# Kernel tuning notes

Measured on AMD Instinct MI355X. Metric: run time of the kernel, lower is better.

Reference implementation:

```python
import jax, jax.numpy as jnp
import numpy as np

P = 8          # patch_num_in == patch_num_out
R = 16         # patch_resolution (pixels per patch side)
C = 2          # dim_channel
D = 512        # dim_token
NH = 8         # nhead
DFF = 2048     # dim_feedforward
L = 6          # num_layers
PAIRS = 5      # demo_num
BS = 8
HW = P * R     # 128
S = PAIRS * 2 * P * P  # 640 tokens
EPS = 1e-5


def _patchify(x):
    # x: (N, c, H, W) -> (N, P*P, c*R*R)
    N, c, H, W = x.shape
    x = x.reshape(N, c, P, R, P, R).transpose(0, 2, 4, 1, 3, 5)
    return x.reshape(N, P * P, c * R * R)


def _depatchify(x, c):
    # x: (N, P*P, c*R*R) -> (N, c, P*R, P*R)
    N = x.shape[0]
    x = x.reshape(N, P, P, c, R, R).transpose(0, 3, 1, 4, 2, 5)
    return x.reshape(N, c, P * R, P * R)


def _ln(x, s, b):
    mu = jnp.mean(x, axis=-1, keepdims=True)
    var = jnp.mean(jnp.square(x - mu), axis=-1, keepdims=True)
    return (x - mu) * jax.lax.rsqrt(var + EPS) * s + b


def _block_lowtri_additive_mask(seq_len):
    blk = jnp.arange(seq_len) // (P * P)  # alternating init/end blocks of size P*P
    allowed = blk[:, None] >= blk[None, :]
    return jnp.where(allowed, 0.0, -jnp.inf).astype(jnp.float32)


def setup_inputs() -> dict:
    key = jax.random.key(0)
    ks = jax.random.split(key, 20)
    s = 0.02
    f32 = jnp.float32
    inp = {
        "init": jax.random.normal(ks[0], (BS, PAIRS, C, HW, HW), f32),
        "end": jax.random.normal(ks[1], (BS, PAIRS, C, HW, HW), f32),
        "c_mask": jnp.ones((BS, C), dtype=bool),
        "pre_W": (jax.random.normal(ks[2], (D, C * R * R), f32) * s),
        "pre_b": jnp.zeros((D,), f32),
        "post_W": (jax.random.normal(ks[3], (C * R * R, D), f32) * s),
        "post_b": jnp.zeros((C * R * R,), f32),
        "patch_pos": jax.random.normal(ks[4], (P * P, D), f32),
        "func_pos": jax.random.normal(ks[5], (PAIRS * 2, D), f32),
        "Wqkv": (jax.random.normal(ks[6], (L, 3 * D, D), f32) * s),
        "bqkv": jnp.zeros((L, 3 * D), f32),
        "Wo": (jax.random.normal(ks[7], (L, D, D), f32) * s),
        "bo": jnp.zeros((L, D), f32),
        "ln1_s": jnp.ones((L, D), f32),
        "ln1_b": jnp.zeros((L, D), f32),
        "ln2_s": jnp.ones((L, D), f32),
        "ln2_b": jnp.zeros((L, D), f32),
        "W1": (jax.random.normal(ks[8], (L, DFF, D), f32) * s),
        "b1": jnp.zeros((L, DFF), f32),
        "W2": (jax.random.normal(ks[9], (L, D, DFF), f32) * s),
        "b2": jnp.zeros((L, D), f32),
    }
    return inp


def _forward(init, end, pre_W, pre_b, post_W, post_b, patch_pos, func_pos,
             Wqkv, bqkv, Wo, bo, ln1_s, ln1_b, ln2_s, ln2_b, W1, b1, W2, b2):
    bs, pairs = init.shape[0], init.shape[1]
    # interleave (init, end) per pair: (bs, pairs, 2, c, h, w)
    x = jnp.concatenate([init[:, :, None], end[:, :, None]], axis=2)
    f = x.reshape(-1, C, HW, HW)
    f = _patchify(f)                                    # (N, P*P, C*R*R)
    f = f @ pre_W.T + pre_b                             # (N, P*P, D)
    f = f + patch_pos                                   # patch pos encoding
    f = f.reshape(bs, pairs * 2, P * P, D)
    f = f + func_pos[: pairs * 2][None, :, None, :]     # func pos encoding
    seq = pairs * 2 * P * P
    f = f.reshape(bs, seq, D)

    amask = _block_lowtri_additive_mask(seq)            # (S, S) additive
    dh = D // NH
    scale = 1.0 / np.sqrt(dh).astype(np.float32)

    for l in range(L):
        qkv = f @ Wqkv[l].T + bqkv[l]                   # (bs, S, 3D)
        q, k, v = jnp.split(qkv, 3, axis=-1)
        q = q.reshape(bs, seq, NH, dh).transpose(0, 2, 1, 3)
        k = k.reshape(bs, seq, NH, dh).transpose(0, 2, 1, 3)
        v = v.reshape(bs, seq, NH, dh).transpose(0, 2, 1, 3)
        scores = jnp.einsum('bhqd,bhkd->bhqk', q, k) * scale + amask
        attn = jax.nn.softmax(scores, axis=-1)
        o = jnp.einsum('bhqk,bhkd->bhqd', attn, v)
        o = o.transpose(0, 2, 1, 3).reshape(bs, seq, D)
        o = o @ Wo[l].T + bo[l]
        f = _ln(f + o, ln1_s[l], ln1_b[l])              # post-norm (PyTorch default)
        ff = jax.nn.gelu(f @ W1[l].T + b1[l], approximate=False) @ W2[l].T + b2[l]
        f = _ln(f + ff, ln2_s[l], ln2_b[l])

    f = f.reshape(bs, pairs, 2, P * P, D)[:, :, 0]      # read prediction off init slots
    f = f @ post_W.T + post_b                           # (bs, pairs, P*P, C*R*R)
    f = f.reshape(bs * pairs, P * P, C * R * R)
    f = _depatchify(f, C)
    return f.reshape(bs, pairs, C, HW, HW)


def reference(init, end, c_mask, pre_W, pre_b, post_W, post_b, patch_pos, func_pos,
              Wqkv, bqkv, Wo, bo, ln1_s, ln1_b, ln2_s, ln2_b, W1, b1, W2, b2):
    # c_mask is unpacked but unused by the original forward
    return _forward(init, end, pre_W, pre_b, post_W, post_b, patch_pos, func_pos,
                    Wqkv, bqkv, Wo, bo, ln1_s, ln1_b, ln2_s, ln2_b, W1, b1, W2, b2)
```

## Files before the change

kernel.cpp:

```cpp
#include <hip/hip_runtime.h>
#include <hip/hip_bf16.h>

#define BSZ 8
#define PAIRS 5
#define NCH 2
#define HWP 128
#define PP 64
#define DIM 512
#define NHEAD 8
#define DHEAD 64
#define DFF 2048
#define NLAYER 6
#define SEQ 640
#define NTOK (BSZ * SEQ)
#define FIN 10
#define MPOST (BSZ * PAIRS * PP)

typedef unsigned short u16;
typedef __bf16 bf16_t;
typedef __attribute__((ext_vector_type(8))) __bf16 bf16x8;
typedef __attribute__((ext_vector_type(8))) unsigned short u16x8;
typedef __attribute__((ext_vector_type(4))) unsigned short u16x4;
typedef __attribute__((ext_vector_type(4))) float f32x4;
#define MFMA16(a, b, c) __builtin_amdgcn_mfma_f32_16x16x32_bf16(a, b, c, 0, 0, 0)

__device__ __forceinline__ u16 f2b(float x) {
  unsigned u = __float_as_uint(x);
  return (u16)((u + 0x7fffu + ((u >> 16) & 1u)) >> 16);
}

__device__ __forceinline__ float gelu_t(float x) {
  float y = 0.7978845608f * (x + 0.044715f * x * x * x);
  y = fminf(fmaxf(y, -10.f), 10.f);
  float e = __expf(2.f * y);
  return 0.5f * x * (1.f + (e - 1.f) / (e + 1.f));
}

__device__ __forceinline__ void dma16(const u16* g, void* l) {
  __builtin_amdgcn_global_load_lds(
      (const __attribute__((address_space(1))) void*)g,
      (__attribute__((address_space(3))) void*)l, 16, 0, 0);
}

#define W_QKV (3 * DIM * DIM)
#define W_O (DIM * DIM)
#define W_1 (DFF * DIM)
#define OFF_O W_QKV
#define OFF_1 (W_QKV + W_O)
#define OFF_2 (W_QKV + W_O + W_1)
#define W_ALL (W_QKV + W_O + 2 * W_1)
#define PREPOST (2 * DIM * DIM)
#define N_CVT (PREPOST + NLAYER * W_ALL)

__global__ __launch_bounds__(256) void k_cvt_all(const float* __restrict__ preW,
                                                 const float* __restrict__ postW,
                                                 const float* __restrict__ wq,
                                                 const float* __restrict__ wo,
                                                 const float* __restrict__ w1,
                                                 const float* __restrict__ w2,
                                                 u16* __restrict__ dst) {
  size_t i = ((size_t)blockIdx.x * 256 + threadIdx.x) * 8;
  const float* src;
  size_t off;
  if (i < DIM * DIM) { src = preW; off = i; }
  else if (i < PREPOST) { src = postW; off = i - DIM * DIM; }
  else {
    size_t j = i - PREPOST;
    int l = (int)(j / W_ALL);
    size_t r = j - (size_t)l * W_ALL;
    if (r < OFF_O) { src = wq + (size_t)l * W_QKV; off = r; }
    else if (r < OFF_1) { src = wo + (size_t)l * W_O; off = r - OFF_O; }
    else if (r < OFF_2) { src = w1 + (size_t)l * W_1; off = r - OFF_1; }
    else { src = w2 + (size_t)l * W_1; off = r - OFF_2; }
  }
  float4 v0 = *(const float4*)(src + off);
  float4 v1 = *(const float4*)(src + off + 4);
  u16x8 o;
  o[0] = f2b(v0.x); o[1] = f2b(v0.y); o[2] = f2b(v0.z); o[3] = f2b(v0.w);
  o[4] = f2b(v1.x); o[5] = f2b(v1.y); o[6] = f2b(v1.z); o[7] = f2b(v1.w);
  *(u16x8*)(dst + i) = o;
}

__global__ __launch_bounds__(256) void k_patchify(const float* __restrict__ init,
                                                  const float* __restrict__ endp,
                                                  u16* __restrict__ A) {
  int i = blockIdx.x * 256 + threadIdx.x;
  int d = i & 511;
  int g = i >> 9;
  int p = g & 63;
  int fi = (g >> 6) % FIN;
  int b = g / SEQ;
  int e = fi & 1;
  int pr = fi >> 1;
  int c = d >> 8;
  int r1 = (d >> 4) & 15;
  int r2 = d & 15;
  int row = ((p >> 3) << 4) + r1;
  int col = ((p & 7) << 4) + r2;
  const float* src = e ? endp : init;
  size_t off = ((size_t)((b * PAIRS + pr) * NCH + c) << 14) + (size_t)row * HWP + col;
  A[i] = f2b(src[off]);
}

template <int BM, int NT, int MODE, int GATHER>
__global__ __launch_bounds__(256) void k_mma(const u16* __restrict__ A,
                                             const u16* __restrict__ B,
                                             const float* __restrict__ bias,
                                             u16* __restrict__ outB,
                                             float* __restrict__ outP,
                                             float* __restrict__ outF,
                                             const float* __restrict__ pp,
                                             const float* __restrict__ fp,
                                             int M, int N, int K, int act) {
  constexpr int FJ = NT / 32;
  constexpr int MI = BM / 32;
  constexpr int ACH = BM / 16;
  constexpr int NC = (BM / 16 + NT / 16) / 4;
  __shared__ __align__(16) bf16_t As[3][BM][32];
  __shared__ __align__(16) bf16_t Bs[3][NT][32];
  const int t = threadIdx.x;
  const int w = t >> 6, lane = t & 63, quad = lane >> 4, l16 = lane & 15;
  int bx = blockIdx.x, by = blockIdx.y;
  if ((gridDim.y & 7) == 0) {
    int lin = bx + gridDim.x * by;
    int YT = gridDim.y >> 3;
    int xcd = lin & 7, slot = lin >> 3;
    by = xcd * YT + slot % YT;
    bx = slot / YT;
  }
  const int row0 = by * BM, col0 = bx * NT;
  const int mB = (w & 1) * (BM / 2);
  const int nB = (w >> 1) * (NT / 2);

  const u16* aP[ACH];
#pragma unroll
  for (int c = 0; c < ACH; ++c) {
    int r = row0 + c * 16 + (lane >> 2);
    int g = r;
    if (GATHER) {
      int p = r & 63, pr = (r >> 6) % PAIRS, b = r / (PAIRS * PP);
      g = b * SEQ + pr * 128 + p;
    }
    aP[c] = A + (size_t)g * K + ((lane & 3) << 3);
  }
  const u16* bP = B + (size_t)(col0 + (lane >> 2)) * K + ((lane & 3) << 3);

  f32x4 acc[MI][FJ];
#pragma unroll
  for (int i = 0; i < MI; ++i)
#pragma unroll
    for (int j = 0; j < FJ; ++j) acc[i][j] = (f32x4){0.f, 0.f, 0.f, 0.f};

  auto stage = [&](int bu, int kk) {
#pragma unroll
    for (int s = 0; s < NC; ++s) {
      int c = NC * w + s;
      if (c < ACH) dma16(aP[c] + kk, &As[bu][c * 16][0]);
      else dma16(bP + (size_t)((c - ACH) * 16) * K + kk, &Bs[bu][(c - ACH) * 16][0]);
    }
  };

  const int iters = K >> 5;
  stage(0, 0);
  stage(1, 32);
  for (int it = 0; it < iters; ++it) {
    const int cur = it % 3;
    if (it > 0) asm volatile("s_barrier" ::: "memory");
    if (it + 2 < iters) stage((it + 2) % 3, (it + 2) << 5);
    if (it + 2 < iters) {
      if constexpr (NC == 2) asm volatile("s_waitcnt vmcnt(4)" ::: "memory");
      else if constexpr (NC == 3) asm volatile("s_waitcnt vmcnt(6)" ::: "memory");
      else asm volatile("s_waitcnt vmcnt(8)" ::: "memory");
    } else if (it + 1 < iters) {
      if constexpr (NC == 2) asm volatile("s_waitcnt vmcnt(2)" ::: "memory");
      else if constexpr (NC == 3) asm volatile("s_waitcnt vmcnt(3)" ::: "memory");
      else asm volatile("s_waitcnt vmcnt(4)" ::: "memory");
    } else {
      asm volatile("s_waitcnt vmcnt(0)" ::: "memory");
    }
    asm volatile("s_barrier" ::: "memory");
    bf16x8 af[MI], bfr[FJ];
#pragma unroll
    for (int i = 0; i < MI; ++i)
      af[i] = *(const bf16x8*)&As[cur][mB + i * 16 + l16][quad * 8];
#pragma unroll
    for (int j = 0; j < FJ; ++j)
      bfr[j] = *(const bf16x8*)&Bs[cur][nB + j * 16 + l16][quad * 8];
#pragma unroll
    for (int i = 0; i < MI; ++i)
#pragma unroll
      for (int j = 0; j < FJ; ++j) acc[i][j] = MFMA16(af[i], bfr[j], acc[i][j]);
  }

#pragma unroll
  for (int i = 0; i < MI; ++i)
#pragma unroll
    for (int reg = 0; reg < 4; ++reg) {
      int m = row0 + mB + i * 16 + quad * 4 + reg;
#pragma unroll
      for (int j = 0; j < FJ; ++j) {
        int n = col0 + nB + j * 16 + l16;
        float v = acc[i][j][reg];
        if (MODE == 0) {
          v += bias[n];
          if (act) v = gelu_t(v);
          outB[(size_t)m * N + n] = f2b(v);
        } else if (MODE == 1) {
          outP[(size_t)m * N + n] = v;
        } else if (MODE == 2) {
          int p = m & 63, fi = (m >> 6) % FIN;
          v += bias[n] + pp[p * DIM + n] + fp[fi * DIM + n];
          outF[(size_t)m * N + n] = v;
          outB[(size_t)m * N + n] = f2b(v);
        } else {
          v += bias[n];
          int p = m & 63, pr = (m >> 6) % PAIRS, b = m / (PAIRS * PP);
          int c = n >> 8, r1 = (n >> 4) & 15, r2 = n & 15;
          int row = ((p >> 3) << 4) + r1, col = ((p & 7) << 4) + r2;
          size_t off = ((size_t)((b * PAIRS + pr) * NCH + c) << 14) +
                       (size_t)row * HWP + col;
          outF[off] = v;
        }
      }
    }
}

__global__ __launch_bounds__(256) void k_attn(const u16* __restrict__ qkv,
                                              u16* __restrict__ o, int qmul) {
  __shared__ bf16_t Qs[64][72];
  __shared__ bf16_t Ks[64][72];
  __shared__ bf16_t Vs[64][72];
  __shared__ bf16_t Ps[64][72];
  const int t = threadIdx.x;
  const int w = t >> 6, lane = t & 63, quad = lane >> 4, l16 = lane & 15;
  const int qblk = blockIdx.x * qmul, h = blockIdx.y, b = blockIdx.z;
  const int q0 = qblk << 6;
  const u16* base = qkv + (size_t)b * SEQ * (3 * DIM);
  const int sr = t >> 2;
  const int sd = (t & 3) << 4;
  const int rowB = 3 * DIM;
  {
    const u16* qp = base + (size_t)(q0 + sr) * rowB + h * DHEAD + sd;
    *(bf16x8*)&Qs[sr][sd] = *(const bf16x8*)(const void*)qp;
    *(bf16x8*)&Qs[sr][sd + 8] = *(const bf16x8*)(const void*)(qp + 8);
  }
  __syncthreads();
  bf16x8 aQ0 = *(const bf16x8*)&Qs[w * 16 + l16][quad * 8];
  bf16x8 aQ1 = *(const bf16x8*)&Qs[w * 16 + l16][32 + quad * 8];
  f32x4 accO[4];
#pragma unroll
  for (int j = 0; j < 4; ++j) accO[j] = (f32x4){0.f, 0.f, 0.f, 0.f};
  float mSt[4] = {-1e30f, -1e30f, -1e30f, -1e30f};
  float lSt[4] = {0.f, 0.f, 0.f, 0.f};
  const int ntile = qblk + 1;
  const u16* kp0 = base + (size_t)sr * rowB + DIM + h * DHEAD + sd;
  const u16* vp0 = base + (size_t)sr * rowB + 2 * DIM + h * DHEAD + sd;
  bf16x8 kR0 = *(const bf16x8*)(const void*)kp0;
  bf16x8 kR1 = *(const bf16x8*)(const void*)(kp0 + 8);
  bf16x8 vR0 = *(const bf16x8*)(const void*)vp0;
  bf16x8 vR1 = *(const bf16x8*)(const void*)(vp0 + 8);
  for (int kt = 0; kt < ntile; ++kt) {
    *(bf16x8*)&Ks[sr][sd] = kR0;
    *(bf16x8*)&Ks[sr][sd + 8] = kR1;
#pragma unroll
    for (int e = 0; e < 8; ++e) Vs[sd + e][sr] = vR0[e];
#pragma unroll
    for (int e = 0; e < 8; ++e) Vs[sd + 8 + e][sr] = vR1[e];
    if (kt + 1 < ntile) {
      const u16* kp = kp0 + (size_t)(kt + 1) * 64 * rowB;
      const u16* vp = vp0 + (size_t)(kt + 1) * 64 * rowB;
      kR0 = *(const bf16x8*)(const void*)kp;
      kR1 = *(const bf16x8*)(const void*)(kp + 8);
      vR0 = *(const bf16x8*)(const void*)vp;
      vR1 = *(const bf16x8*)(const void*)(vp + 8);
    }
    __syncthreads();
    f32x4 s[4];
#pragma unroll
    for (int j = 0; j < 4; ++j) {
      bf16x8 b0 = *(const bf16x8*)&Ks[j * 16 + l16][quad * 8];
      bf16x8 b1 = *(const bf16x8*)&Ks[j * 16 + l16][32 + quad * 8];
      s[j] = (f32x4){0.f, 0.f, 0.f, 0.f};
      s[j] = MFMA16(aQ0, b0, s[j]);
      s[j] = MFMA16(aQ1, b1, s[j]);
      s[j] *= 0.125f;
    }
#pragma unroll
    for (int reg = 0; reg < 4; ++reg) {
      float mx = fmaxf(fmaxf(s[0][reg], s[1][reg]), fmaxf(s[2][reg], s[3][reg]));
      mx = fmaxf(mx, __shfl_xor(mx, 1));
      mx = fmaxf(mx, __shfl_xor(mx, 2));
      mx = fmaxf(mx, __shfl_xor(mx, 4));
      mx = fmaxf(mx, __shfl_xor(mx, 8));
      float mNew = fmaxf(mSt[reg], mx);
      float alpha = __expf(mSt[reg] - mNew);
      mSt[reg] = mNew;
      float rs = 0.f;
#pragma unroll
      for (int j = 0; j < 4; ++j) {
        float p = __expf(s[j][reg] - mNew);
        s[j][reg] = p;
        rs += p;
      }
      rs += __shfl_xor(rs, 1);
      rs += __shfl_xor(rs, 2);
      rs += __shfl_xor(rs, 4);
      rs += __shfl_xor(rs, 8);
      lSt[reg] = lSt[reg] * alpha + rs;
#pragma unroll
      for (int j = 0; j < 4; ++j) accO[j][reg] *= alpha;
    }
#pragma unroll
    for (int j = 0; j < 4; ++j)
#pragma unroll
      for (int reg = 0; reg < 4; ++reg)
        *(u16*)&Ps[w * 16 + quad * 4 + reg][j * 16 + l16] = f2b(s[j][reg]);
    __syncthreads();
    bf16x8 aP0 = *(const bf16x8*)&Ps[w * 16 + l16][quad * 8];
    bf16x8 aP1 = *(const bf16x8*)&Ps[w * 16 + l16][32 + quad * 8];
#pragma unroll
    for (int jd = 0; jd < 4; ++jd) {
      bf16x8 b0 = *(const bf16x8*)&Vs[jd * 16 + l16][quad * 8];
      bf16x8 b1 = *(const bf16x8*)&Vs[jd * 16 + l16][32 + quad * 8];
      accO[jd] = MFMA16(aP0, b0, accO[jd]);
      accO[jd] = MFMA16(aP1, b1, accO[jd]);
    }
    __syncthreads();
  }
#pragma unroll
  for (int reg = 0; reg < 4; ++reg) {
    float inv = 1.0f / lSt[reg];
    int row = q0 + w * 16 + quad * 4 + reg;
#pragma unroll
    for (int jd = 0; jd < 4; ++jd)
      o[((size_t)(b * SEQ + row)) * DIM + h * DHEAD + jd * 16 + l16] =
          f2b(accO[jd][reg] * inv);
  }
}

template <int GIN>
__global__ __launch_bounds__(256) void k_red_ln(const float* __restrict__ part,
                                                const float* __restrict__ bias,
                                                const float* __restrict__ f_in,
                                                float* __restrict__ f_out,
                                                u16* __restrict__ fb_out,
                                                const float* __restrict__ s,
                                                const float* __restrict__ bvec) {
  const int t = threadIdx.x;
  const int half = t >> 7;
  const int r = blockIdx.x * 2 + half;
  const int c = (t & 127) * 4;
  int g = r;
  if (GIN) {
    int p = r & 63, pr = (r >> 6) % PAIRS, b = r / (PAIRS * PP);
    g = b * SEQ + pr * 128 + p;
  }
  float4 x = *(const float4*)(f_in + (size_t)g * DIM + c);
  float4 pa = *(const float4*)(part + (size_t)r * DIM + c);
  float4 bi = *(const float4*)(bias + c);
  x.x += pa.x + bi.x; x.y += pa.y + bi.y; x.z += pa.z + bi.z; x.w += pa.w + bi.w;
  float sum = x.x + x.y + x.z + x.w;
  float sq = x.x * x.x + x.y * x.y + x.z * x.z + x.w * x.w;
#pragma unroll
  for (int off = 32; off; off >>= 1) {
    sum += __shfl_xor(sum, off);
    sq += __shfl_xor(sq, off);
  }
  __shared__ float rs[4], rq[4];
  const int w = t >> 6, lane = t & 63;
  if (lane == 0) { rs[w] = sum; rq[w] = sq; }
  __syncthreads();
  float tot = rs[half * 2] + rs[half * 2 + 1];
  float tq2 = rq[half * 2] + rq[half * 2 + 1];
  float mu = tot * (1.0f / 512.0f);
  float var = tq2 * (1.0f / 512.0f) - mu * mu;
  float rstd = rsqrtf(var + 1e-5f);
  float4 sv = *(const float4*)(s + c);
  float4 bv = *(const float4*)(bvec + c);
  float4 o;
  o.x = (x.x - mu) * rstd * sv.x + bv.x;
  o.y = (x.y - mu) * rstd * sv.y + bv.y;
  o.z = (x.z - mu) * rstd * sv.z + bv.z;
  o.w = (x.w - mu) * rstd * sv.w + bv.w;
  *(float4*)(f_out + (size_t)r * DIM + c) = o;
  u16x4 ob;
  ob[0] = f2b(o.x); ob[1] = f2b(o.y); ob[2] = f2b(o.z); ob[3] = f2b(o.w);
  *(u16x4*)(fb_out + (size_t)r * DIM + c) = ob;
}

extern "C" void kernel_launch(void* const* d_in, const int* in_sizes, int n_in,
                              void* d_out, int out_size, void* d_ws, size_t ws_size,
                              hipStream_t stream) {
  const float* init = (const float*)d_in[0];
  const float* endp = (const float*)d_in[1];
  const float* pre_W = (const float*)d_in[3];
  const float* pre_b = (const float*)d_in[4];
  const float* post_W = (const float*)d_in[5];
  const float* post_b = (const float*)d_in[6];
  const float* patch_pos = (const float*)d_in[7];
  const float* func_pos = (const float*)d_in[8];
  const float* Wqkv = (const float*)d_in[9];
  const float* bqkv = (const float*)d_in[10];
  const float* Wo = (const float*)d_in[11];
  const float* bo = (const float*)d_in[12];
  const float* ln1_s = (const float*)d_in[13];
  const float* ln1_b = (const float*)d_in[14];
  const float* ln2_s = (const float*)d_in[15];
  const float* ln2_b = (const float*)d_in[16];
  const float* W1 = (const float*)d_in[17];
  const float* b1 = (const float*)d_in[18];
  const float* W2 = (const float*)d_in[19];
  const float* b2 = (const float*)d_in[20];
  float* out = (float*)d_out;

  char* p = (char*)d_ws;
  float* buf_f = (float*)p;    p += (size_t)NTOK * DIM * 4;
  u16* buf_fb = (u16*)p;       p += (size_t)NTOK * DIM * 2;
  u16* buf_attn = (u16*)p;     p += (size_t)NTOK * DIM * 2;
  u16* shared_b = (u16*)p;     p += (size_t)NTOK * DFF * 2;
  u16* wAll = (u16*)p;         p += (size_t)N_CVT * 2;
  float* partial = (float*)p;  p += (size_t)NTOK * DIM * 4;
  float* buf_fc = (float*)p;   p += (size_t)MPOST * DIM * 4;
  u16* buf_fbc = (u16*)p;      p += (size_t)MPOST * DIM * 2;
  u16* buf_patch = shared_b;
  u16* buf_qkv = shared_b;
  u16* buf_hid = shared_b;
  u16* wPre = wAll;
  u16* wPost = wAll + DIM * DIM;
  u16* wL = wAll + PREPOST;

  dim3 blk(256);
  const int elems = NTOK * DIM;

  k_cvt_all<<<N_CVT / (256 * 8), blk, 0, stream>>>(pre_W, post_W, Wqkv, Wo, W1, W2,
                                                   wAll);
  k_patchify<<<elems / 256, blk, 0, stream>>>(init, endp, buf_patch);
  k_mma<64, 128, 2, 0><<<dim3(4, 80), blk, 0, stream>>>(
      buf_patch, wPre, pre_b, buf_fb, nullptr, buf_f, patch_pos, func_pos,
      NTOK, DIM, DIM, 0);

  for (int l = 0; l < NLAYER; ++l) {
    u16* wB = wL + (size_t)l * W_ALL;
    k_mma<128, 128, 0, 0><<<dim3(12, 40), blk, 0, stream>>>(
        buf_fb, wB, bqkv + (size_t)l * 3 * DIM, buf_qkv, nullptr, nullptr, nullptr,
        nullptr, NTOK, 3 * DIM, DIM, 0);
    if (l < NLAYER - 1) {
      k_attn<<<dim3(SEQ / 64, NHEAD, BSZ), blk, 0, stream>>>(buf_qkv, buf_attn, 1);
      k_mma<64, 128, 1, 0><<<dim3(4, 80), blk, 0, stream>>>(
          buf_attn, wB + OFF_O, nullptr, nullptr, partial, nullptr, nullptr, nullptr,
          NTOK, DIM, DIM, 0);
      k_red_ln<0><<<NTOK / 2, blk, 0, stream>>>(partial, bo + (size_t)l * DIM,
                                                buf_f, buf_f, buf_fb,
                                                ln1_s + (size_t)l * DIM,
                                                ln1_b + (size_t)l * DIM);
      k_mma<128, 128, 0, 0><<<dim3(16, 40), blk, 0, stream>>>(
          buf_fb, wB + OFF_1, b1 + (size_t)l * DFF, buf_hid, nullptr, nullptr,
          nullptr, nullptr, NTOK, DFF, DIM, 1);
      k_mma<64, 128, 1, 0><<<dim3(4, 80), blk, 0, stream>>>(
          buf_hid, wB + OFF_2, nullptr, nullptr, partial, nullptr, nullptr, nullptr,
          NTOK, DIM, DFF, 0);
      k_red_ln<0><<<NTOK / 2, blk, 0, stream>>>(partial, b2 + (size_t)l * DIM,
                                                buf_f, buf_f, buf_fb,
                                                ln2_s + (size_t)l * DIM,
                                                ln2_b + (size_t)l * DIM);
    } else {
      k_attn<<<dim3(SEQ / 128, NHEAD, BSZ), blk, 0, stream>>>(buf_qkv, buf_attn, 2);
      k_mma<64, 64, 1, 1><<<dim3(8, 40), blk, 0, stream>>>(
          buf_attn, wB + OFF_O, nullptr, nullptr, partial, nullptr, nullptr, nullptr,
          MPOST, DIM, DIM, 0);
      k_red_ln<1><<<MPOST / 2, blk, 0, stream>>>(partial, bo + (size_t)l * DIM,
                                                 buf_f, buf_fc, buf_fbc,
                                                 ln1_s + (size_t)l * DIM,
                                                 ln1_b + (size_t)l * DIM);
      k_mma<128, 128, 0, 0><<<dim3(16, 20), blk, 0, stream>>>(
          buf_fbc, wB + OFF_1, b1 + (size_t)l * DFF, buf_hid, nullptr, nullptr,
          nullptr, nullptr, MPOST, DFF, DIM, 1);
      k_mma<64, 64, 1, 0><<<dim3(8, 40), blk, 0, stream>>>(
          buf_hid, wB + OFF_2, nullptr, nullptr, partial, nullptr, nullptr, nullptr,
          MPOST, DIM, DFF, 0);
      k_red_ln<0><<<MPOST / 2, blk, 0, stream>>>(partial, b2 + (size_t)l * DIM,
                                                 buf_fc, buf_fc, buf_fbc,
                                                 ln2_s + (size_t)l * DIM,
                                                 ln2_b + (size_t)l * DIM);
    }
  }

  k_mma<64, 64, 3, 0><<<dim3(8, 40), blk, 0, stream>>>(
      buf_fbc, wPost, post_b, nullptr, nullptr, out, nullptr, nullptr,
      MPOST, DIM, DIM, 0);
}
```

Measured before the change: 909.0 us.

## Fuse residual add and LayerNorm into full-row output-projection GEMM epilogue

Adds a k_mma_ln kernel in which each block computes a 64x512 output tile covering the whole row, then adds bias and residual and applies LayerNorm in the epilogue, with a cross-wave reduction through shared memory. This removes the separate k_red_ln launches and the fp32 partial buffer round-trip after the Wo and W2 projections. Other GEMM launches switch to 64-row tiles to double the block count. The fused kernel has only NTOK/64 = 80 blocks and a large LDS footprint, so occupancy and parallelism are reduced in exchange for less memory traffic.

```diff
diff --git a/kernel.cpp b/kernel.cpp
--- a/kernel.cpp
+++ b/kernel.cpp
@@ -40,6 +40,16 @@
   __builtin_amdgcn_global_load_lds(
       (const __attribute__((address_space(1))) void*)g,
       (__attribute__((address_space(3))) void*)l, 16, 0, 0);
+}
+
+template <int N> __device__ __forceinline__ void vwait() {
+  if constexpr (N == 0) asm volatile("s_waitcnt vmcnt(0)" ::: "memory");
+  else if constexpr (N == 2) asm volatile("s_waitcnt vmcnt(2)" ::: "memory");
+  else if constexpr (N == 3) asm volatile("s_waitcnt vmcnt(3)" ::: "memory");
+  else if constexpr (N == 4) asm volatile("s_waitcnt vmcnt(4)" ::: "memory");
+  else if constexpr (N == 6) asm volatile("s_waitcnt vmcnt(6)" ::: "memory");
+  else if constexpr (N == 9) asm volatile("s_waitcnt vmcnt(9)" ::: "memory");
+  else if constexpr (N == 18) asm volatile("s_waitcnt vmcnt(18)" ::: "memory");
 }
 
 #define W_QKV (3 * DIM * DIM)
@@ -167,17 +177,9 @@
     const int cur = it % 3;
     if (it > 0) asm volatile("s_barrier" ::: "memory");
     if (it + 2 < iters) stage((it + 2) % 3, (it + 2) << 5);
-    if (it + 2 < iters) {
-      if constexpr (NC == 2) asm volatile("s_waitcnt vmcnt(4)" ::: "memory");
-      else if constexpr (NC == 3) asm volatile("s_waitcnt vmcnt(6)" ::: "memory");
-      else asm volatile("s_waitcnt vmcnt(8)" ::: "memory");
-    } else if (it + 1 < iters) {
-      if constexpr (NC == 2) asm volatile("s_waitcnt vmcnt(2)" ::: "memory");
-      else if constexpr (NC == 3) asm volatile("s_waitcnt vmcnt(3)" ::: "memory");
-      else asm volatile("s_waitcnt vmcnt(4)" ::: "memory");
-    } else {
-      asm volatile("s_waitcnt vmcnt(0)" ::: "memory");
-    }
+    if (it + 2 < iters) vwait<2 * NC>();
+    else if (it + 1 < iters) vwait<NC>();
+    else vwait<0>();
     asm volatile("s_barrier" ::: "memory");
     bf16x8 af[MI], bfr[FJ];
 #pragma unroll
@@ -225,6 +227,127 @@
     }
 }
 
+template <int GATHER, int GIN>
+__global__ __launch_bounds__(256) void k_mma_ln(const u16* __restrict__ A,
+                                               const u16* __restrict__ B,
+                                               const float* __restrict__ bias,
+                                               const float* __restrict__ f_in,
+                                               float* __restrict__ f_out,
+                                               u16* __restrict__ fb_out,
+                                               const float* __restrict__ sc,
+                                               const float* __restrict__ bv,
+                                               int M, int K) {
+  constexpr int FJ = 16;
+  constexpr int MI = 2;
+  constexpr int NC = 9;
+  __shared__ __align__(16) bf16_t As[3][64][32];
+  __shared__ __align__(16) bf16_t Bs[3][512][32];
+  __shared__ float redS[2][64], redQ[2][64];
+  const int t = threadIdx.x;
+  const int w = t >> 6, lane = t & 63, quad = lane >> 4, l16 = lane & 15;
+  const int row0 = blockIdx.x * 64;
+  const int mB = (w & 1) * 32;
+  const int nB = (w >> 1) * 256;
+
+  const u16* aP[4];
+#pragma unroll
+  for (int c = 0; c < 4; ++c) {
+    int r = row0 + c * 16 + (lane >> 2);
+    int g = r;
+    if (GATHER) {
+      int p = r & 63, pr = (r >> 6) % PAIRS, b = r / (PAIRS * PP);
+      g = b * SEQ + pr * 128 + p;
+    }
+    aP[c] = A + (size_t)g * K + ((lane & 3) << 3);
+  }
+  const u16* bP = B + (size_t)(lane >> 2) * K + ((lane & 3) << 3);
+
+  f32x4 acc[MI][FJ];
+#pragma unroll
+  for (int i = 0; i < MI; ++i)
+#pragma unroll
+    for (int j = 0; j < FJ; ++j) acc[i][j] = (f32x4){0.f, 0.f, 0.f, 0.f};
+
+  auto stage = [&](int bu, int kk) {
+#pragma unroll
+    for (int s = 0; s < NC; ++s) {
+      int c = NC * w + s;
+      if (c < 4) dma16(aP[c] + kk, &As[bu][c * 16][0]);
+      else dma16(bP + (size_t)((c - 4) * 16) * K + kk, &Bs[bu][(c - 4) * 16][0]);
+    }
+  };
+
+  const int iters = K >> 5;
+  stage(0, 0);
+  stage(1, 32);
+  for (int it = 0; it < iters; ++it) {
+    const int cur = it % 3;
+    if (it > 0) asm volatile("s_barrier" ::: "memory");
+    if (it + 2 < iters) stage((it + 2) % 3, (it + 2) << 5);
+    if (it + 2 < iters) vwait<18>();
+    else if (it + 1 < iters) vwait<9>();
+    else vwait<0>();
+    asm volatile("s_barrier" ::: "memory");
+    bf16x8 af[MI];
+#pragma unroll
+    for (int i = 0; i < MI; ++i)
+      af[i] = *(const bf16x8*)&As[cur][mB + i * 16 + l16][quad * 8];
+#pragma unroll
+    for (int j = 0; j < FJ; ++j) {
+      bf16x8 bb = *(const bf16x8*)&Bs[cur][nB + j * 16 + l16][quad * 8];
+#pragma unroll
+      for (int i = 0; i < MI; ++i) acc[i][j] = MFMA16(af[i], bb, acc[i][j]);
+    }
+  }
+
+#pragma unroll
+  for (int i = 0; i < MI; ++i)
+#pragma unroll
+    for (int reg = 0; reg < 4; ++reg) {
+      const int ml = mB + i * 16 + quad * 4 + reg;
+      int r = row0 + ml;
+      int g = r;
+      if (GIN) {
+        int p = r & 63, pr = (r >> 6) % PAIRS, b = r / (PAIRS * PP);
+        g = b * SEQ + pr * 128 + p;
+      }
+      float s_ = 0.f, q_ = 0.f;
+#pragma unroll
+      for (int j = 0; j < FJ; ++j) {
+        int n = nB + j * 16 + l16;
+        float v = acc[i][j][reg] + bias[n] + f_in[(size_t)g * DIM + n];
+        acc[i][j][reg] = v;
+        s_ += v;
+        q_ += v * v;
+      }
+      s_ += __shfl_xor(s_, 1); q_ += __shfl_xor(q_, 1);
+      s_ += __shfl_xor(s_, 2); q_ += __shfl_xor(q_, 2);
+      s_ += __shfl_xor(s_, 4); q_ += __shfl_xor(q_, 4);
+      s_ += __shfl_xor(s_, 8); q_ += __shfl_xor(q_, 8);
+      if (l16 == 0) { redS[w >> 1][ml] = s_; redQ[w >> 1][ml] = q_; }
+    }
+  __syncthreads();
+#pragma unroll
+  for (int i = 0; i < MI; ++i)
+#pragma unroll
+    for (int reg = 0; reg < 4; ++reg) {
+      const int ml = mB + i * 16 + quad * 4 + reg;
+      const int r = row0 + ml;
+      float tot = redS[0][ml] + redS[1][ml];
+      float tq = redQ[0][ml] + redQ[1][ml];
+      float mu = tot * (1.0f / 512.0f);
+      float var = tq * (1.0f / 512.0f) - mu * mu;
+      float rstd = rsqrtf(var + 1e-5f);
+#pragma unroll
+      for (int j = 0; j < FJ; ++j) {
+        int n = nB + j * 16 + l16;
+        float o = (acc[i][j][reg] - mu) * rstd * sc[n] + bv[n];
+        f_out[(size_t)r * DIM + n] = o;
+        fb_out[(size_t)r * DIM + n] = f2b(o);
+      }
+    }
+}
+
 __global__ __launch_bounds__(256) void k_attn(const u16* __restrict__ qkv,
                                               u16* __restrict__ o, int qmul) {
   __shared__ bf16_t Qs[64][72];
@@ -336,56 +459,6 @@
       o[((size_t)(b * SEQ + row)) * DIM + h * DHEAD + jd * 16 + l16] =
           f2b(accO[jd][reg] * inv);
   }
-}
-
-template <int GIN>
-__global__ __launch_bounds__(256) void k_red_ln(const float* __restrict__ part,
-                                                const float* __restrict__ bias,
-                                                const float* __restrict__ f_in,
-                                                float* __restrict__ f_out,
-                                                u16* __restrict__ fb_out,
-                                                const float* __restrict__ s,
-                                                const float* __restrict__ bvec) {
-  const int t = threadIdx.x;
-  const int half = t >> 7;
-  const int r = blockIdx.x * 2 + half;
-  const int c = (t & 127) * 4;
-  int g = r;
-  if (GIN) {
-    int p = r & 63, pr = (r >> 6) % PAIRS, b = r / (PAIRS * PP);
-    g = b * SEQ + pr * 128 + p;
-  }
-  float4 x = *(const float4*)(f_in + (size_t)g * DIM + c);
-  float4 pa = *(const float4*)(part + (size_t)r * DIM + c);
-  float4 bi = *(const float4*)(bias + c);
-  x.x += pa.x + bi.x; x.y += pa.y + bi.y; x.z += pa.z + bi.z; x.w += pa.w + bi.w;
-  float sum = x.x + x.y + x.z + x.w;
-  float sq = x.x * x.x + x.y * x.y + x.z * x.z + x.w * x.w;
-#pragma unroll
-  for (int off = 32; off; off >>= 1) {
-    sum += __shfl_xor(sum, off);
-    sq += __shfl_xor(sq, off);
-  }
-  __shared__ float rs[4], rq[4];
-  const int w = t >> 6, lane = t & 63;
-  if (lane == 0) { rs[w] = sum; rq[w] = sq; }
-  __syncthreads();
-  float tot = rs[half * 2] + rs[half * 2 + 1];
-  float tq2 = rq[half * 2] + rq[half * 2 + 1];
-  float mu = tot * (1.0f / 512.0f);
-  float var = tq2 * (1.0f / 512.0f) - mu * mu;
-  float rstd = rsqrtf(var + 1e-5f);
-  float4 sv = *(const float4*)(s + c);
-  float4 bv = *(const float4*)(bvec + c);
-  float4 o;
-  o.x = (x.x - mu) * rstd * sv.x + bv.x;
-  o.y = (x.y - mu) * rstd * sv.y + bv.y;
-  o.z = (x.z - mu) * rstd * sv.z + bv.z;
-  o.w = (x.w - mu) * rstd * sv.w + bv.w;
-  *(float4*)(f_out + (size_t)r * DIM + c) = o;
-  u16x4 ob;
-  ob[0] = f2b(o.x); ob[1] = f2b(o.y); ob[2] = f2b(o.z); ob[3] = f2b(o.w);
-  *(u16x4*)(fb_out + (size_t)r * DIM + c) = ob;
 }
 
 extern "C" void kernel_launch(void* const* d_in, const int* in_sizes, int n_in,
@@ -428,6 +501,7 @@
   u16* wPre = wAll;
   u16* wPost = wAll + DIM * DIM;
   u16* wL = wAll + PREPOST;
+  (void)partial;
 
   dim3 blk(256);
   const int elems = NTOK * DIM;
@@ -435,53 +509,37 @@
   k_cvt_all<<<N_CVT / (256 * 8), blk, 0, stream>>>(pre_W, post_W, Wqkv, Wo, W1, W2,
                                                    wAll);
   k_patchify<<<elems / 256, blk, 0, stream>>>(init, endp, buf_patch);
-  k_mma<64, 128, 2, 0><<<dim3(4, 80), blk, 0, stream>>>(
+  k_mma<64, 64, 2, 0><<<dim3(8, 80), blk, 0, stream>>>(
       buf_patch, wPre, pre_b, buf_fb, nullptr, buf_f, patch_pos, func_pos,
       NTOK, DIM, DIM, 0);
 
   for (int l = 0; l < NLAYER; ++l) {
     u16* wB = wL + (size_t)l * W_ALL;
-    k_mma<128, 128, 0, 0><<<dim3(12, 40), blk, 0, stream>>>(
+    k_mma<64, 128, 0, 0><<<dim3(12, 80), blk, 0, stream>>>(
         buf_fb, wB, bqkv + (size_t)l * 3 * DIM, buf_qkv, nullptr, nullptr, nullptr,
         nullptr, NTOK, 3 * DIM, DIM, 0);
     if (l < NLAYER - 1) {
       k_attn<<<dim3(SEQ / 64, NHEAD, BSZ), blk, 0, stream>>>(buf_qkv, buf_attn, 1);
-      k_mma<64, 128, 1, 0><<<dim3(4, 80), blk, 0, stream>>>(
-          buf_attn, wB + OFF_O, nullptr, nullptr, partial, nullptr, nullptr, nullptr,
-          NTOK, DIM, DIM, 0);
-      k_red_ln<0><<<NTOK / 2, blk, 0, stream>>>(partial, bo + (size_t)l * DIM,
-                                                buf_f, buf_f, buf_fb,
-                                                ln1_s + (size_t)l * DIM,
-                                                ln1_b + (size_t)l * DIM);
-      k_mma<128, 128, 0, 0><<<dim3(16, 40), blk, 0, stream>>>(
+      k_mma_ln<0, 0><<<dim3(NTOK / 64), blk, 0, stream>>>(
+          buf_attn, wB + OFF_O, bo + (size_t)l * DIM, buf_f, buf_f, buf_fb,
+          ln1_s + (size_t)l * DIM, ln1_b + (size_t)l * DIM, NTOK, DIM);
+      k_mma<64, 128, 0, 0><<<dim3(16, 80), blk, 0, stream>>>(
           buf_fb, wB + OFF_1, b1 + (size_t)l * DFF, buf_hid, nullptr, nullptr,
           nullptr, nullptr, NTOK, DFF, DIM, 1);
-      k_mma<64, 128, 1, 0><<<dim3(4, 80), blk, 0, stream>>>(
-          buf_hid, wB + OFF_2, nullptr, nullptr, partial, nullptr, nullptr, nullptr,
-          NTOK, DIM, DFF, 0);
-      k_red_ln<0><<<NTOK / 2, blk, 0, stream>>>(partial, b2 + (size_t)l * DIM,
-                                                buf_f, buf_f, buf_fb,
-                                                ln2_s + (size_t)l * DIM,
-                                                ln2_b + (size_t)l * DIM);
+      k_mma_ln<0, 0><<<dim3(NTOK / 64), blk, 0, stream>>>(
+          buf_hid, wB + OFF_2, b2 + (size_t)l * DIM, buf_f, buf_f, buf_fb,
+          ln2_s + (size_t)l * DIM, ln2_b + (size_t)l * DIM, NTOK, DFF);
     } else {
       k_attn<<<dim3(SEQ / 128, NHEAD, BSZ), blk, 0, stream>>>(buf_qkv, buf_attn, 2);
-      k_mma<64, 64, 1, 1><<<dim3(8, 40), blk, 0, stream>>>(
-          buf_attn, wB + OFF_O, nullptr, nullptr, partial, nullptr, nullptr, nullptr,
-          MPOST, DIM, DIM, 0);
-      k_red_ln<1><<<MPOST / 2, blk, 0, stream>>>(partial, bo + (size_t)l * DIM,
-                                                 buf_f, buf_fc, buf_fbc,
-                                                 ln1_s + (size_t)l * DIM,
-                                                 ln1_b + (size_t)l * DIM);
-      k_mma<128, 128, 0, 0><<<dim3(16, 20), blk, 0, stream>>>(
+      k_mma_ln<1, 1><<<dim3(MPOST / 64), blk, 0, stream>>>(
+          buf_attn, wB + OFF_O, bo + (size_t)l * DIM, buf_f, buf_fc, buf_fbc,
+          ln1_s + (size_t)l * DIM, ln1_b + (size_t)l * DIM, MPOST, DIM);
+      k_mma<64, 128, 0, 0><<<dim3(16, 40), blk, 0, stream>>>(
           buf_fbc, wB + OFF_1, b1 + (size_t)l * DFF, buf_hid, nullptr, nullptr,
           nullptr, nullptr, MPOST, DFF, DIM, 1);
-      k_mma<64, 64, 1, 0><<<dim3(8, 40), blk, 0, stream>>>(
-          buf_hid, wB + OFF_2, nullptr, nullptr, partial, nullptr, nullptr, nullptr,
-          MPOST, DIM, DFF, 0);
-      k_red_ln<0><<<MPOST / 2, blk, 0, stream>>>(partial, b2 + (size_t)l * DIM,
-                                                 buf_fc, buf_fc, buf_fbc,
-                                                 ln2_s + (size_t)l * DIM,
-                                                 ln2_b + (size_t)l * DIM);
+      k_mma_ln<0, 0><<<dim3(MPOST / 64), blk, 0, stream>>>(
+          buf_hid, wB + OFF_2, b2 + (size_t)l * DIM, buf_fc, buf_fc, buf_fbc,
+          ln2_s + (size_t)l * DIM, ln2_b + (size_t)l * DIM, MPOST, DFF);
     }
   }
 
```

After: 1.330 ms. +46.3%, slower.
